# Kernel tuning notes

Measured on AMD Instinct MI355X. Metric: run time of the kernel, lower is better.

The kernel has to match this reference:

```python
import jax, jax.numpy as jnp
import numpy as np


def setup_inputs() -> dict:
    key = jax.random.key(0)
    ks = jax.random.split(key, 13)
    B, D, H, O = 4096, 2048, 3, 1  # batch, input_dim, hidden layer count, output_dim
    f32 = jnp.float32
    scale = 1.0 / np.sqrt(D)
    return {
        "x": jax.random.normal(ks[0], (B, D), f32),
        "w_mu_h": jax.random.normal(ks[1], (H, D, D), f32) * scale,
        "w_rho_h": jax.random.normal(ks[2], (H, D, D), f32) - 5.0,  # softplus(-5) ~ small std
        "b_mu_h": jax.random.normal(ks[3], (H, D), f32) * scale,
        "b_rho_h": jax.random.normal(ks[4], (H, D), f32) - 5.0,
        "w_mu_o": jax.random.normal(ks[5], (O, D), f32) * scale,
        "w_rho_o": jax.random.normal(ks[6], (O, D), f32) - 5.0,
        "b_mu_o": jax.random.normal(ks[7], (O,), f32) * scale,
        "b_rho_o": jax.random.normal(ks[8], (O,), f32) - 5.0,
        # reparameterization noise (torch.randn_like), passed explicitly for determinism
        "eps_w_h": jax.random.normal(ks[9], (H, D, D), f32),
        "eps_b_h": jax.random.normal(ks[10], (H, D), f32),
        "eps_w_o": jax.random.normal(ks[11], (O, D), f32),
        "eps_b_o": jax.random.normal(ks[12], (O,), f32),
    }


def _vlinear(x, w_mu, w_rho, b_mu, b_rho, eps_w, eps_b):
    # weight = mu + eps * softplus(rho); F.linear(x, W, b) = x @ W.T + b
    w = w_mu + eps_w * jax.nn.softplus(w_rho)
    b = b_mu + eps_b * jax.nn.softplus(b_rho)
    return x @ w.T + b


def reference(x, w_mu_h, w_rho_h, b_mu_h, b_rho_h,
              w_mu_o, w_rho_o, b_mu_o, b_rho_o,
              eps_w_h, eps_b_h, eps_w_o, eps_b_o):
    def step(h, p):
        wm, wr, bm, br, ew, eb = p
        h = jax.nn.relu(_vlinear(h, wm, wr, bm, br, ew, eb))
        return h, None

    h, _ = jax.lax.scan(step, x, (w_mu_h, w_rho_h, b_mu_h, b_rho_h, eps_w_h, eps_b_h))
    return _vlinear(h, w_mu_o, w_rho_o, b_mu_o, b_rho_o, eps_w_o, eps_b_o)
```

## Files before the change

kernel.cpp:

```cpp
#include <hip/hip_runtime.h>

#define BB 4096
#define DD 2048

typedef float f32x4 __attribute__((ext_vector_type(4)));
typedef __bf16 bf16x8 __attribute__((ext_vector_type(8)));

typedef __attribute__((address_space(1))) unsigned int gl_u32;
typedef __attribute__((address_space(3))) unsigned int lds_u32;

#define GLOAD_LDS16(gptr, sptr) \
  __builtin_amdgcn_global_load_lds((gl_u32*)(void*)(gptr), (lds_u32*)(sptr), 16, 0, 0)

__device__ __forceinline__ unsigned short f2bf(float f) {
  unsigned int u = __float_as_uint(f);
  u += 0x7fffu + ((u >> 16) & 1u);
  return (unsigned short)(u >> 16);
}

__device__ __forceinline__ float sp(float x) {
  float t = __expf(-fabsf(x));
  return fmaxf(x, 0.0f) + __logf(1.0f + t);
}

__device__ __forceinline__ void prep_w_vec4(
    const float* __restrict__ mu, const float* __restrict__ rho,
    const float* __restrict__ eps, unsigned short* __restrict__ Wh,
    long long i)
{
  float4 m = ((const float4*)mu)[i];
  float4 r = ((const float4*)rho)[i];
  float4 e = ((const float4*)eps)[i];
  ushort4 o;
  o.x = f2bf(m.x + e.x * sp(r.x));
  o.y = f2bf(m.y + e.y * sp(r.y));
  o.z = f2bf(m.z + e.z * sp(r.z));
  o.w = f2bf(m.w + e.w * sp(r.w));
  ((ushort4*)Wh)[i] = o;
}

__device__ __forceinline__ void prep_f32_vec4(
    const float* __restrict__ mu, const float* __restrict__ rho,
    const float* __restrict__ eps, float* __restrict__ out, long long i)
{
  float4 m = ((const float4*)mu)[i];
  float4 r = ((const float4*)rho)[i];
  float4 e = ((const float4*)eps)[i];
  float4 o;
  o.x = m.x + e.x * sp(r.x);
  o.y = m.y + e.y * sp(r.y);
  o.z = m.z + e.z * sp(r.z);
  o.w = m.w + e.w * sp(r.w);
  ((float4*)out)[i] = o;
}

__global__ __launch_bounds__(512) void prep0_kernel(
    const float* __restrict__ x,
    const float* __restrict__ wmuh, const float* __restrict__ wrhoh,
    const float* __restrict__ bmuh, const float* __restrict__ brhoh,
    const float* __restrict__ epswh, const float* __restrict__ epsbh,
    unsigned short* __restrict__ Wh, unsigned short* __restrict__ Xb,
    float* __restrict__ bh)
{
  const int b = blockIdx.x;
  const int t = threadIdx.x;
  if (b < 512) {
    long long base = (long long)b * 2048 + t;
    #pragma unroll
    for (int j = 0; j < 4; ++j)
      prep_w_vec4(wmuh, wrhoh, epswh, Wh, base + j * 512);
    return;
  }
  if (b < 1536) {
    long long base = (long long)(b - 512) * 2048 + t;
    #pragma unroll
    for (int j = 0; j < 4; ++j) {
      float4 v = ((const float4*)x)[base + j * 512];
      ushort4 o;
      o.x = f2bf(v.x); o.y = f2bf(v.y); o.z = f2bf(v.z); o.w = f2bf(v.w);
      ((ushort4*)Xb)[base + j * 512] = o;
    }
    return;
  }
  prep_f32_vec4(bmuh, brhoh, epsbh, bh, t);
}

#define NGEMM 512

struct GemmCoords { int m0, n0, mw, nw; int srow[2], sgc[2]; };

__device__ __forceinline__ GemmCoords gemm_coords(int id, int t) {
  GemmCoords g;
  const int w = t >> 6;
  const int p = id & 7;
  const int i4 = id >> 3;
  const int mt = (p & 3) * 8 + (i4 & 7);
  const int nt = (p >> 2) * 8 + (i4 >> 3);
  g.m0 = mt * 128;
  g.n0 = nt * 128;
  g.mw = (w >> 2) * 64;
  g.nw = (w & 3) * 32;
  #pragma unroll
  for (int i = 0; i < 2; ++i) {
    int c = i * 512 + t;
    g.srow[i] = c >> 3;
    g.sgc[i] = (c & 7) ^ (g.srow[i] & 7);
  }
  return g;
}

__device__ __forceinline__ void gemm_mainloop(
    const unsigned short* __restrict__ A,
    const unsigned short* __restrict__ W,
    unsigned short* sA, unsigned short* sB,
    const GemmCoords& gc, int t, f32x4 (&acc)[4][2])
{
  const int K = DD;
  const int l = t & 63;
  const int lq = l >> 4;
  const int lr = l & 15;
  for (int kt = 0; kt < K; kt += 64) {
    #pragma unroll
    for (int i = 0; i < 2; ++i) {
      int c = i * 512 + t;
      const unsigned short* ga = A + (size_t)(gc.m0 + gc.srow[i]) * K + kt + gc.sgc[i] * 8;
      GLOAD_LDS16(ga, &sA[c * 8]);
      const unsigned short* gb = W + (size_t)(gc.n0 + gc.srow[i]) * K + kt + gc.sgc[i] * 8;
      GLOAD_LDS16(gb, &sB[c * 8]);
    }
    __syncthreads();

    #pragma unroll
    for (int s = 0; s < 2; ++s) {
      bf16x8 af[4], bfr[2];
      int g = s * 4 + lq;
      #pragma unroll
      for (int i = 0; i < 4; ++i) {
        int ra = gc.mw + i * 16 + lr;
        af[i] = *(const bf16x8*)&sA[ra * 64 + (g ^ (ra & 7)) * 8];
      }
      #pragma unroll
      for (int j = 0; j < 2; ++j) {
        int rb = gc.nw + j * 16 + lr;
        bfr[j] = *(const bf16x8*)&sB[rb * 64 + (g ^ (rb & 7)) * 8];
      }
      #pragma unroll
      for (int i = 0; i < 4; ++i)
        #pragma unroll
        for (int j = 0; j < 2; ++j)
          acc[i][j] = __builtin_amdgcn_mfma_f32_16x16x32_bf16(af[i], bfr[j], acc[i][j], 0, 0, 0);
    }
    __syncthreads();
  }
}

__device__ __forceinline__ void gemm_epilogue_store(
    const GemmCoords& gc, int t, f32x4 (&acc)[4][2],
    const float* __restrict__ bias, unsigned short* __restrict__ C)
{
  const int N = DD;
  const int l = t & 63;
  const int lq = l >> 4;
  const int lr = l & 15;
  #pragma unroll
  for (int j = 0; j < 2; ++j) {
    int n = gc.n0 + gc.nw + j * 16 + lr;
    float bv = bias[n];
    #pragma unroll
    for (int i = 0; i < 4; ++i) {
      int mbase = gc.m0 + gc.mw + i * 16 + lq * 4;
      #pragma unroll
      for (int r = 0; r < 4; ++r) {
        float v = fmaxf(acc[i][j][r] + bv, 0.0f);
        C[(size_t)(mbase + r) * N + n] = f2bf(v);
      }
    }
  }
}

__global__ __launch_bounds__(512, 4) void gemm_relu_fused_kernel(
    const unsigned short* __restrict__ A,
    const unsigned short* __restrict__ W,
    const float* __restrict__ bias,
    unsigned short* __restrict__ C,
    const float* __restrict__ wmuh, const float* __restrict__ wrhoh,
    const float* __restrict__ bmuh, const float* __restrict__ brhoh,
    const float* __restrict__ wmuo, const float* __restrict__ wrhoo,
    const float* __restrict__ epswh, const float* __restrict__ epsbh,
    const float* __restrict__ epswo,
    unsigned short* __restrict__ Wh, float* __restrict__ bh,
    float* __restrict__ wo)
{
  __shared__ unsigned short sA[128 * 64];
  __shared__ unsigned short sB[128 * 64];

  const int id = blockIdx.x;
  const int t = threadIdx.x;

  if (id >= NGEMM) {
    const int pb = id - NGEMM;
    if (pb < 1024) {
      long long base = 1048576LL + (long long)pb * 2048 + t;
      #pragma unroll
      for (int j = 0; j < 4; ++j)
        prep_w_vec4(wmuh, wrhoh, epswh, Wh, base + j * 512);
      return;
    }
    #pragma unroll
    for (int j = 0; j < 2; ++j)
      prep_f32_vec4(bmuh, brhoh, epsbh, bh, 512 + j * 512 + t);
    prep_f32_vec4(wmuo, wrhoo, epswo, wo, t);
    return;
  }

  GemmCoords gc = gemm_coords(id, t);
  f32x4 acc[4][2] = {};
  gemm_mainloop(A, W, sA, sB, gc, t, acc);
  gemm_epilogue_store(gc, t, acc, bias, C);
}

__global__ __launch_bounds__(512, 4) void gemm_relu_kernel(
    const unsigned short* __restrict__ A,
    const unsigned short* __restrict__ W,
    const float* __restrict__ bias,
    unsigned short* __restrict__ C)
{
  __shared__ unsigned short sA[128 * 64];
  __shared__ unsigned short sB[128 * 64];
  const int t = threadIdx.x;
  GemmCoords gc = gemm_coords(blockIdx.x, t);
  f32x4 acc[4][2] = {};
  gemm_mainloop(A, W, sA, sB, gc, t, acc);
  gemm_epilogue_store(gc, t, acc, bias, C);
}

__global__ __launch_bounds__(512, 4) void gemm_relu_dot_kernel(
    const unsigned short* __restrict__ A,
    const unsigned short* __restrict__ W,
    const float* __restrict__ bias,
    const float* __restrict__ wo,
    float* __restrict__ Pbuf)
{
  __shared__ unsigned short sA[128 * 64];
  __shared__ unsigned short sB[128 * 64];
  const int t = threadIdx.x;

  GemmCoords gc = gemm_coords(blockIdx.x, t);
  f32x4 acc[4][2] = {};
  gemm_mainloop(A, W, sA, sB, gc, t, acc);

  const int l = t & 63;
  const int w = t >> 6;
  const int lq = l >> 4;
  const int lr = l & 15;
  const int nq = w & 3;

  float bv[2], wv[2];
  #pragma unroll
  for (int j = 0; j < 2; ++j) {
    int n = gc.n0 + gc.nw + j * 16 + lr;
    bv[j] = bias[n];
    wv[j] = wo[n];
  }
  float partial[4][4];
  #pragma unroll
  for (int i = 0; i < 4; ++i)
    #pragma unroll
    for (int r = 0; r < 4; ++r)
      partial[i][r] = fmaxf(acc[i][0][r] + bv[0], 0.0f) * wv[0]
                    + fmaxf(acc[i][1][r] + bv[1], 0.0f) * wv[1];

  #pragma unroll
  for (int d = 1; d <= 8; d <<= 1)
    #pragma unroll
    for (int i = 0; i < 4; ++i)
      #pragma unroll
      for (int r = 0; r < 4; ++r)
        partial[i][r] += __shfl_xor(partial[i][r], d, 64);

  float* sRed = (float*)sA;
  if (lr == 0) {
    #pragma unroll
    for (int i = 0; i < 4; ++i)
      #pragma unroll
      for (int r = 0; r < 4; ++r) {
        int row = gc.mw + i * 16 + lq * 4 + r;
        sRed[row * 4 + nq] = partial[i][r];
      }
  }
  __syncthreads();
  if (t < 128) {
    float s = sRed[t * 4 + 0] + sRed[t * 4 + 1] + sRed[t * 4 + 2] + sRed[t * 4 + 3];
    int nt = gc.n0 >> 7;
    Pbuf[nt * BB + gc.m0 + t] = s;
  }
}

__global__ __launch_bounds__(256) void reduce_out_kernel(
    const float* __restrict__ Pbuf,
    const float* __restrict__ bmuo, const float* __restrict__ brhoo,
    const float* __restrict__ epsbo,
    float* __restrict__ out)
{
  const int m = blockIdx.x * 256 + threadIdx.x;
  float s = bmuo[0] + epsbo[0] * sp(brhoo[0]);
  #pragma unroll
  for (int nt = 0; nt < 16; ++nt)
    s += Pbuf[nt * BB + m];
  out[m] = s;
}

extern "C" void kernel_launch(void* const* d_in, const int* in_sizes, int n_in,
                              void* d_out, int out_size, void* d_ws, size_t ws_size,
                              hipStream_t stream) {
  const float* x     = (const float*)d_in[0];
  const float* wmuh  = (const float*)d_in[1];
  const float* wrhoh = (const float*)d_in[2];
  const float* bmuh  = (const float*)d_in[3];
  const float* brhoh = (const float*)d_in[4];
  const float* wmuo  = (const float*)d_in[5];
  const float* wrhoo = (const float*)d_in[6];
  const float* bmuo  = (const float*)d_in[7];
  const float* brhoo = (const float*)d_in[8];
  const float* epswh = (const float*)d_in[9];
  const float* epsbh = (const float*)d_in[10];
  const float* epswo = (const float*)d_in[11];
  const float* epsbo = (const float*)d_in[12];

  char* ws = (char*)d_ws;
  unsigned short* Wh = (unsigned short*)(ws);
  unsigned short* Xb = (unsigned short*)(ws + 25165824);
  unsigned short* Ha = (unsigned short*)(ws + 25165824 + 16777216);
  unsigned short* Hb = (unsigned short*)(ws + 25165824 + 2 * 16777216);
  float* bh   = (float*)(ws + 25165824 + 3 * 16777216);
  float* wo   = (float*)(ws + 25165824 + 3 * 16777216 + 24576);
  float* Pbuf = (float*)(ws + 25165824 + 3 * 16777216 + 24576 + 8192);

  prep0_kernel<<<1537, 512, 0, stream>>>(
      x, wmuh, wrhoh, bmuh, brhoh, epswh, epsbh, Wh, Xb, bh);

  gemm_relu_fused_kernel<<<NGEMM + 1025, 512, 0, stream>>>(
      Xb, Wh, bh, Ha,
      wmuh, wrhoh, bmuh, brhoh, wmuo, wrhoo,
      epswh, epsbh, epswo, Wh, bh, wo);

  gemm_relu_kernel<<<NGEMM, 512, 0, stream>>>(Ha, Wh + 1 * 4194304, bh + DD, Hb);

  gemm_relu_dot_kernel<<<NGEMM, 512, 0, stream>>>(
      Hb, Wh + 2 * 4194304, bh + 2 * DD, wo, Pbuf);

  reduce_out_kernel<<<BB / 256, 256, 0, stream>>>(
      Pbuf, bmuo, brhoo, epsbo, (float*)d_out);
}
```

Before: 298.3 us.

## Use 4-wave 64x64 warp tiles and fuse final reduction via last-block atomic counter

The GEMM blocks go from 8 waves with 64x32 warp tiles to 4 waves with 64x64 warp tiles. This raises register-level fragment reuse and cuts LDS reads per MFMA, at the cost of more accumulator registers and fewer waves per block. The separate reduce_out kernel is removed: the last GEMM block to finish, found through an atomic counter that the prep kernel zeroes, sums the partial buffer and writes the output. That saves one launch but leaves the final reduction serialized on a single block.

After: 332.9 us. 11.6% more time.

```diff
diff --git a/kernel.cpp b/kernel.cpp
--- a/kernel.cpp
+++ b/kernel.cpp
@@ -60,7 +60,7 @@
     const float* __restrict__ bmuh, const float* __restrict__ brhoh,
     const float* __restrict__ epswh, const float* __restrict__ epsbh,
     unsigned short* __restrict__ Wh, unsigned short* __restrict__ Xb,
-    float* __restrict__ bh)
+    float* __restrict__ bh, unsigned int* __restrict__ counter)
 {
   const int b = blockIdx.x;
   const int t = threadIdx.x;
@@ -83,11 +83,12 @@
     return;
   }
   prep_f32_vec4(bmuh, brhoh, epsbh, bh, t);
+  if (t == 0) *counter = 0u;
 }
 
 #define NGEMM 512
 
-struct GemmCoords { int m0, n0, mw, nw; int srow[2], sgc[2]; };
+struct GemmCoords { int m0, n0, mw, nw; int srow[4], sgc[4]; };
 
 __device__ __forceinline__ GemmCoords gemm_coords(int id, int t) {
   GemmCoords g;
@@ -98,11 +99,11 @@
   const int nt = (p >> 2) * 8 + (i4 >> 3);
   g.m0 = mt * 128;
   g.n0 = nt * 128;
-  g.mw = (w >> 2) * 64;
-  g.nw = (w & 3) * 32;
-  #pragma unroll
-  for (int i = 0; i < 2; ++i) {
-    int c = i * 512 + t;
+  g.mw = (w >> 1) * 64;
+  g.nw = (w & 1) * 64;
+  #pragma unroll
+  for (int i = 0; i < 4; ++i) {
+    int c = i * 256 + t;
     g.srow[i] = c >> 3;
     g.sgc[i] = (c & 7) ^ (g.srow[i] & 7);
   }
@@ -113,7 +114,7 @@
     const unsigned short* __restrict__ A,
     const unsigned short* __restrict__ W,
     unsigned short* sA, unsigned short* sB,
-    const GemmCoords& gc, int t, f32x4 (&acc)[4][2])
+    const GemmCoords& gc, int t, f32x4 (&acc)[4][4])
 {
   const int K = DD;
   const int l = t & 63;
@@ -121,8 +122,8 @@
   const int lr = l & 15;
   for (int kt = 0; kt < K; kt += 64) {
     #pragma unroll
-    for (int i = 0; i < 2; ++i) {
-      int c = i * 512 + t;
+    for (int i = 0; i < 4; ++i) {
+      int c = i * 256 + t;
       const unsigned short* ga = A + (size_t)(gc.m0 + gc.srow[i]) * K + kt + gc.sgc[i] * 8;
       GLOAD_LDS16(ga, &sA[c * 8]);
       const unsigned short* gb = W + (size_t)(gc.n0 + gc.srow[i]) * K + kt + gc.sgc[i] * 8;
@@ -132,22 +133,19 @@
 
     #pragma unroll
     for (int s = 0; s < 2; ++s) {
-      bf16x8 af[4], bfr[2];
+      bf16x8 af[4], bfr[4];
       int g = s * 4 + lq;
       #pragma unroll
       for (int i = 0; i < 4; ++i) {
         int ra = gc.mw + i * 16 + lr;
         af[i] = *(const bf16x8*)&sA[ra * 64 + (g ^ (ra & 7)) * 8];
-      }
-      #pragma unroll
-      for (int j = 0; j < 2; ++j) {
-        int rb = gc.nw + j * 16 + lr;
-        bfr[j] = *(const bf16x8*)&sB[rb * 64 + (g ^ (rb & 7)) * 8];
+        int rb = gc.nw + i * 16 + lr;
+        bfr[i] = *(const bf16x8*)&sB[rb * 64 + (g ^ (rb & 7)) * 8];
       }
       #pragma unroll
       for (int i = 0; i < 4; ++i)
         #pragma unroll
-        for (int j = 0; j < 2; ++j)
+        for (int j = 0; j < 4; ++j)
           acc[i][j] = __builtin_amdgcn_mfma_f32_16x16x32_bf16(af[i], bfr[j], acc[i][j], 0, 0, 0);
     }
     __syncthreads();
@@ -155,7 +153,7 @@
 }
 
 __device__ __forceinline__ void gemm_epilogue_store(
-    const GemmCoords& gc, int t, f32x4 (&acc)[4][2],
+    const GemmCoords& gc, int t, f32x4 (&acc)[4][4],
     const float* __restrict__ bias, unsigned short* __restrict__ C)
 {
   const int N = DD;
@@ -163,7 +161,7 @@
   const int lq = l >> 4;
   const int lr = l & 15;
   #pragma unroll
-  for (int j = 0; j < 2; ++j) {
+  for (int j = 0; j < 4; ++j) {
     int n = gc.n0 + gc.nw + j * 16 + lr;
     float bv = bias[n];
     #pragma unroll
@@ -178,7 +176,7 @@
   }
 }
 
-__global__ __launch_bounds__(512, 4) void gemm_relu_fused_kernel(
+__global__ __launch_bounds__(256, 2) void gemm_relu_fused_kernel(
     const unsigned short* __restrict__ A,
     const unsigned short* __restrict__ W,
     const float* __restrict__ bias,
@@ -202,24 +200,26 @@
     if (pb < 1024) {
       long long base = 1048576LL + (long long)pb * 2048 + t;
       #pragma unroll
-      for (int j = 0; j < 4; ++j)
-        prep_w_vec4(wmuh, wrhoh, epswh, Wh, base + j * 512);
+      for (int j = 0; j < 8; ++j)
+        prep_w_vec4(wmuh, wrhoh, epswh, Wh, base + j * 256);
       return;
     }
     #pragma unroll
+    for (int j = 0; j < 4; ++j)
+      prep_f32_vec4(bmuh, brhoh, epsbh, bh, 512 + j * 256 + t);
+    #pragma unroll
     for (int j = 0; j < 2; ++j)
-      prep_f32_vec4(bmuh, brhoh, epsbh, bh, 512 + j * 512 + t);
-    prep_f32_vec4(wmuo, wrhoo, epswo, wo, t);
+      prep_f32_vec4(wmuo, wrhoo, epswo, wo, j * 256 + t);
     return;
   }
 
   GemmCoords gc = gemm_coords(id, t);
-  f32x4 acc[4][2] = {};
+  f32x4 acc[4][4] = {};
   gemm_mainloop(A, W, sA, sB, gc, t, acc);
   gemm_epilogue_store(gc, t, acc, bias, C);
 }
 
-__global__ __launch_bounds__(512, 4) void gemm_relu_kernel(
+__global__ __launch_bounds__(256, 2) void gemm_relu_kernel(
     const unsigned short* __restrict__ A,
     const unsigned short* __restrict__ W,
     const float* __restrict__ bias,
@@ -229,35 +229,39 @@
   __shared__ unsigned short sB[128 * 64];
   const int t = threadIdx.x;
   GemmCoords gc = gemm_coords(blockIdx.x, t);
-  f32x4 acc[4][2] = {};
+  f32x4 acc[4][4] = {};
   gemm_mainloop(A, W, sA, sB, gc, t, acc);
   gemm_epilogue_store(gc, t, acc, bias, C);
 }
 
-__global__ __launch_bounds__(512, 4) void gemm_relu_dot_kernel(
+__global__ __launch_bounds__(256, 2) void gemm_relu_dot_kernel(
     const unsigned short* __restrict__ A,
     const unsigned short* __restrict__ W,
     const float* __restrict__ bias,
     const float* __restrict__ wo,
-    float* __restrict__ Pbuf)
+    float* __restrict__ Pbuf,
+    unsigned int* __restrict__ counter,
+    const float* __restrict__ bmuo, const float* __restrict__ brhoo,
+    const float* __restrict__ epsbo,
+    float* __restrict__ out)
 {
   __shared__ unsigned short sA[128 * 64];
   __shared__ unsigned short sB[128 * 64];
+  __shared__ int s_last;
   const int t = threadIdx.x;
 
   GemmCoords gc = gemm_coords(blockIdx.x, t);
-  f32x4 acc[4][2] = {};
+  f32x4 acc[4][4] = {};
   gemm_mainloop(A, W, sA, sB, gc, t, acc);
 
   const int l = t & 63;
   const int w = t >> 6;
   const int lq = l >> 4;
   const int lr = l & 15;
-  const int nq = w & 3;
-
-  float bv[2], wv[2];
-  #pragma unroll
-  for (int j = 0; j < 2; ++j) {
+
+  float bv[4], wv[4];
+  #pragma unroll
+  for (int j = 0; j < 4; ++j) {
     int n = gc.n0 + gc.nw + j * 16 + lr;
     bv[j] = bias[n];
     wv[j] = wo[n];
@@ -266,9 +270,13 @@
   #pragma unroll
   for (int i = 0; i < 4; ++i)
     #pragma unroll
-    for (int r = 0; r < 4; ++r)
-      partial[i][r] = fmaxf(acc[i][0][r] + bv[0], 0.0f) * wv[0]
-                    + fmaxf(acc[i][1][r] + bv[1], 0.0f) * wv[1];
+    for (int r = 0; r < 4; ++r) {
+      float v = 0.0f;
+      #pragma unroll
+      for (int j = 0; j < 4; ++j)
+        v += fmaxf(acc[i][j][r] + bv[j], 0.0f) * wv[j];
+      partial[i][r] = v;
+    }
 
   #pragma unroll
   for (int d = 1; d <= 8; d <<= 1)
@@ -285,29 +293,36 @@
       #pragma unroll
       for (int r = 0; r < 4; ++r) {
         int row = gc.mw + i * 16 + lq * 4 + r;
-        sRed[row * 4 + nq] = partial[i][r];
+        sRed[row * 2 + (w & 1)] = partial[i][r];
       }
   }
   __syncthreads();
   if (t < 128) {
-    float s = sRed[t * 4 + 0] + sRed[t * 4 + 1] + sRed[t * 4 + 2] + sRed[t * 4 + 3];
+    float s = sRed[t * 2 + 0] + sRed[t * 2 + 1];
     int nt = gc.n0 >> 7;
     Pbuf[nt * BB + gc.m0 + t] = s;
   }
-}
-
-__global__ __launch_bounds__(256) void reduce_out_kernel(
-    const float* __restrict__ Pbuf,
-    const float* __restrict__ bmuo, const float* __restrict__ brhoo,
-    const float* __restrict__ epsbo,
-    float* __restrict__ out)
-{
-  const int m = blockIdx.x * 256 + threadIdx.x;
-  float s = bmuo[0] + epsbo[0] * sp(brhoo[0]);
-  #pragma unroll
-  for (int nt = 0; nt < 16; ++nt)
-    s += Pbuf[nt * BB + m];
-  out[m] = s;
+
+  __threadfence();
+  __syncthreads();
+  if (t == 0) {
+    unsigned int old = atomicAdd(counter, 1u);
+    s_last = (old == NGEMM - 1) ? 1 : 0;
+  }
+  __syncthreads();
+  if (s_last) {
+    __threadfence();
+    float bo = bmuo[0] + epsbo[0] * sp(brhoo[0]);
+    #pragma unroll
+    for (int j = 0; j < 16; ++j) {
+      int m = j * 256 + t;
+      float s = bo;
+      #pragma unroll
+      for (int nt = 0; nt < 16; ++nt)
+        s += Pbuf[nt * BB + m];
+      out[m] = s;
+    }
+  }
 }
 
 extern "C" void kernel_launch(void* const* d_in, const int* in_sizes, int n_in,
@@ -335,20 +350,19 @@
   float* bh   = (float*)(ws + 25165824 + 3 * 16777216);
   float* wo   = (float*)(ws + 25165824 + 3 * 16777216 + 24576);
   float* Pbuf = (float*)(ws + 25165824 + 3 * 16777216 + 24576 + 8192);
+  unsigned int* counter = (unsigned int*)(ws + 25165824 + 3 * 16777216 + 24576 + 8192 + 262144);
 
   prep0_kernel<<<1537, 512, 0, stream>>>(
-      x, wmuh, wrhoh, bmuh, brhoh, epswh, epsbh, Wh, Xb, bh);
-
-  gemm_relu_fused_kernel<<<NGEMM + 1025, 512, 0, stream>>>(
+      x, wmuh, wrhoh, bmuh, brhoh, epswh, epsbh, Wh, Xb, bh, counter);
+
+  gemm_relu_fused_kernel<<<NGEMM + 1025, 256, 0, stream>>>(
       Xb, Wh, bh, Ha,
       wmuh, wrhoh, bmuh, brhoh, wmuo, wrhoo,
       epswh, epsbh, epswo, Wh, bh, wo);
 
-  gemm_relu_kernel<<<NGEMM, 512, 0, stream>>>(Ha, Wh + 1 * 4194304, bh + DD, Hb);
-
-  gemm_relu_dot_kernel<<<NGEMM, 512, 0, stream>>>(
-      Hb, Wh + 2 * 4194304, bh + 2 * DD, wo, Pbuf);
-
-  reduce_out_kernel<<<BB / 256, 256, 0, stream>>>(
-      Pbuf, bmuo, brhoo, epsbo, (float*)d_out);
-}
+  gemm_relu_kernel<<<NGEMM, 256, 0, stream>>>(Ha, Wh + 1 * 4194304, bh + DD, Hb);
+
+  gemm_relu_dot_kernel<<<NGEMM, 256, 0, stream>>>(
+      Hb, Wh + 2 * 4194304, bh + 2 * DD, wo, Pbuf,
+      counter, bmuo, brhoo, epsbo, (float*)d_out);
+}
```
